# Kernel optimization log

Hardware: AMD Instinct MI355X
Metric: run time of the kernel (lower is better)

Reference implementation:

```python
import jax, jax.numpy as jnp
import numpy as np

N_NODES = 50000
N_EDGES = 1600000
D_IN = 128
D_HID = 128
D_OUT = 128


def setup_inputs() -> dict:
    key = jax.random.key(0)
    ks = jax.random.split(key, 12)
    s = 0.05
    return {
        "x": jax.random.normal(ks[0], (N_NODES, D_IN), jnp.float32),
        "src": jax.random.randint(ks[1], (N_EDGES,), 0, N_NODES),
        "dst": jax.random.randint(ks[2], (N_EDGES,), 0, N_NODES),
        "W_neigh1": jax.random.normal(ks[3], (D_HID, D_IN), jnp.float32) * s,
        "W_self1": jax.random.normal(ks[4], (D_HID, D_IN), jnp.float32) * s,
        "b_self1": jnp.zeros((D_HID,), jnp.float32),
        "W_neigh2": jax.random.normal(ks[5], (D_HID, D_HID), jnp.float32) * s,
        "W_self2": jax.random.normal(ks[6], (D_HID, D_HID), jnp.float32) * s,
        "b_self2": jnp.zeros((D_HID,), jnp.float32),
        "W_neigh3": jax.random.normal(ks[7], (D_OUT, D_HID), jnp.float32) * s,
        "W_self3": jax.random.normal(ks[8], (D_OUT, D_HID), jnp.float32) * s,
        "b_self3": jnp.zeros((D_OUT,), jnp.float32),
    }


def _sage_mean(h, src, dst, inv_deg, W_neigh, W_self, b_self):
    # DGL SAGEConv 'mean': fc_self(h) + fc_neigh(mean of in-neighbor feats)
    # zero in-degree nodes get zero neighbor term (inv_deg = 0 there is avoided
    # by clamping degree to >=1, sum is 0 anyway).
    neigh_sum = jax.ops.segment_sum(h[src], dst, num_segments=h.shape[0])  # [N, d]
    h_neigh = neigh_sum * inv_deg  # [N, d]
    return h @ W_self.T + b_self + h_neigh @ W_neigh.T


def reference(x, src, dst, W_neigh1, W_self1, b_self1, W_neigh2, W_self2, b_self2, W_neigh3, W_self3, b_self3):
    n = x.shape[0]
    deg = jax.ops.segment_sum(jnp.ones((src.shape[0],), x.dtype), dst, num_segments=n)
    inv_deg = (1.0 / jnp.maximum(deg, 1.0))[:, None]  # [N, 1]
    h = jax.nn.relu(_sage_mean(x, src, dst, inv_deg, W_neigh1, W_self1, b_self1))
    h = jax.nn.relu(_sage_mean(h, src, dst, inv_deg, W_neigh2, W_self2, b_self2))
    h = _sage_mean(h, src, dst, inv_deg, W_neigh3, W_self3, b_self3)
    return h
```

## Files before the change

kernel.cpp:

```cpp
#include <hip/hip_runtime.h>


constexpr int N_NODES = 50000;
constexpr int N_EDGES = 1600000;
constexpr int D = 128;

constexpr int NBUCK = 392;
constexpr int BCAP  = 6144;
constexpr int EPB   = 4096;
constexpr int CS_BLOCKS = (N_EDGES + EPB - 1) / EPB;
constexpr int GC_STRIDE = 16;

constexpr int NT  = 8;
constexpr int TSH = 13;

typedef __bf16 bf16x8 __attribute__((ext_vector_type(8)));
typedef float f32x4 __attribute__((ext_vector_type(4)));
union U8 { bf16x8 v; __bf16 e[8]; };

__global__ void zero1(int* __restrict__ a, int n) {
    int i = blockIdx.x * blockDim.x + threadIdx.x;
    if (i < n) a[i] = 0;
}

__global__ __launch_bounds__(256) void bucket_count_scatter(
        const int* __restrict__ dst, const int* __restrict__ src,
        int* __restrict__ gcursor, int* __restrict__ bucketbuf) {
    __shared__ int hcnt[NBUCK];
    __shared__ int hbase[NBUCK];
    const int tid = threadIdx.x;
    for (int i = tid; i < NBUCK; i += 256) hcnt[i] = 0;
    __syncthreads();

    const int e0 = blockIdx.x * EPB;
    int d[16], lp[16];
    #pragma unroll
    for (int t = 0; t < 16; ++t) {
        const int e = e0 + t * 256 + tid;
        if (e < N_EDGES) {
            d[t] = dst[e];
            lp[t] = atomicAdd(&hcnt[d[t] >> 7], 1);
        } else {
            d[t] = 0; lp[t] = -1;
        }
    }
    __syncthreads();

    for (int i = tid; i < NBUCK; i += 256) {
        const int c = hcnt[i];
        hbase[i] = c ? atomicAdd(&gcursor[i * GC_STRIDE], c) : 0;
    }
    __syncthreads();

    #pragma unroll
    for (int t = 0; t < 16; ++t) {
        const int e = e0 + t * 256 + tid;
        if (e < N_EDGES) {
            const int s  = src[e];
            const int bk = d[t] >> 7;
            const int p  = hbase[bk] + lp[t];
            if (p < BCAP)
                bucketbuf[bk * BCAP + p] = ((d[t] & 127) << 16) | s;
        }
    }
}

__global__ void bucket_scan(const int* __restrict__ gcursor,
                            int* __restrict__ bucket_base) {
    __shared__ int wsum[8], wpre[8];
    const int t = threadIdx.x;
    const int lane = t & 63, w = t >> 6;
    int v = 0;
    if (t < NBUCK) { v = gcursor[t * GC_STRIDE]; if (v > BCAP) v = BCAP; }
    int x = v;
    #pragma unroll
    for (int off = 1; off < 64; off <<= 1) {
        int tt = __shfl_up(x, off, 64);
        if (lane >= off) x += tt;
    }
    if (lane == 63) wsum[w] = x;
    __syncthreads();
    if (t < 8) {
        int s = wsum[t], y = s;
        #pragma unroll
        for (int off = 1; off < 8; off <<= 1) {
            int tt = __shfl_up(y, off, 64);
            if (t >= off) y += tt;
        }
        wpre[t] = y - s;
    }
    __syncthreads();
    if (t < NBUCK) bucket_base[t] = wpre[w] + (x - v);
}

__global__ __launch_bounds__(256) void bucket_csr(
        const int* __restrict__ gcursor, const int* __restrict__ bucket_base,
        const int* __restrict__ bucketbuf, int* __restrict__ tp,
        float* __restrict__ inv_deg, int* __restrict__ esrc) {
    __shared__ int h[1024];
    __shared__ int cur[1024];
    __shared__ int wsum[4], wpre[4];
    const int bk = blockIdx.x, tid = threadIdx.x;
    int cnt = gcursor[bk * GC_STRIDE];
    if (cnt > BCAP) cnt = BCAP;
    const int base = bucket_base[bk];
    #pragma unroll
    for (int k = 0; k < 4; ++k) h[tid * 4 + k] = 0;
    __syncthreads();

    const int* bb = bucketbuf + (size_t)bk * BCAP;
    for (int i = tid; i < cnt; i += 256) {
        const int p = bb[i];
        atomicAdd(&h[((p >> 16) << 3) | ((p & 0xFFFF) >> TSH)], 1);
    }
    __syncthreads();

    if (tid < 128) {
        int dg = 0;
        #pragma unroll
        for (int k = 0; k < 8; ++k) dg += h[tid * 8 + k];
        inv_deg[bk * 128 + tid] = 1.0f / fmaxf((float)dg, 1.0f);
    }

    const int v0 = h[tid * 4], v1 = h[tid * 4 + 1];
    const int v2 = h[tid * 4 + 2], v3 = h[tid * 4 + 3];
    const int s = v0 + v1 + v2 + v3;
    int x = s;
    const int lane = tid & 63, w = tid >> 6;
    #pragma unroll
    for (int off = 1; off < 64; off <<= 1) {
        int tt = __shfl_up(x, off, 64);
        if (lane >= off) x += tt;
    }
    if (lane == 63) wsum[w] = x;
    __syncthreads();
    if (tid == 0) {
        int a = 0;
        #pragma unroll
        for (int k = 0; k < 4; ++k) { wpre[k] = a; a += wsum[k]; }
    }
    __syncthreads();
    const int e0 = wpre[w] + (x - s);
    const int e1 = e0 + v0, e2 = e1 + v1, e3 = e2 + v2;
    cur[tid * 4] = e0; cur[tid * 4 + 1] = e1;
    cur[tid * 4 + 2] = e2; cur[tid * 4 + 3] = e3;
    int* tpo = tp + (size_t)bk * 1024 + tid * 4;
    tpo[0] = base + e0; tpo[1] = base + e1; tpo[2] = base + e2; tpo[3] = base + e3;
    __syncthreads();

    for (int i = tid; i < cnt; i += 256) {
        const int p = bb[i];
        const int f = ((p >> 16) << 3) | ((p & 0xFFFF) >> TSH);
        esrc[base + atomicAdd(&cur[f], 1)] = p & 0xFFFF;
    }
}

__global__ void pack_w(const float* __restrict__ w0, const float* __restrict__ w1,
                       const float* __restrict__ w2, const float* __restrict__ w3,
                       const float* __restrict__ w4, const float* __restrict__ w5,
                       __bf16* __restrict__ outbase) {
    const float* ws[6] = {w0, w1, w2, w3, w4, w5};
    const float* W = ws[blockIdx.y];
    __bf16* o = outbase + (size_t)blockIdx.y * 32768;
    int idx = blockIdx.x * 256 + threadIdx.x;
    int t = idx & 7;
    int lane = (idx >> 3) & 63;
    int ks = (idx >> 9) & 3;
    int jt = idx >> 11;
    int j = jt * 16 + (lane & 15);
    int k = ks * 32 + (lane >> 4) * 8 + t;
    float w = W[j * D + k];
    __bf16 hi = (__bf16)w;
    o[idx] = hi;
    o[16384 + idx] = (__bf16)(w - (float)hi);
}

__global__ __launch_bounds__(256) void dual_gemm(
        const float* __restrict__ h, const __bf16* __restrict__ Bs,
        const __bf16* __restrict__ Bn, const float* __restrict__ bias,
        float* __restrict__ y_self, __bf16* __restrict__ z) {
    const int wave = threadIdx.x >> 6;
    const int lane = threadIdx.x & 63;
    const int tile = blockIdx.x * 4 + wave;
    if (tile >= N_NODES / 16) return;
    const int n0 = tile * 16;
    const int row = n0 + (lane & 15);
    const int koff = (lane >> 4) * 8;

    U8 ahi[4], alo[4];
    #pragma unroll
    for (int ks = 0; ks < 4; ++ks) {
        const float* p = h + (size_t)row * D + ks * 32 + koff;
        float f[8];
        *(f32x4*)&f[0] = *(const f32x4*)p;
        *(f32x4*)&f[4] = *(const f32x4*)(p + 4);
        #pragma unroll
        for (int t = 0; t < 8; ++t) {
            __bf16 hi = (__bf16)f[t];
            ahi[ks].e[t] = hi;
            alo[ks].e[t] = (__bf16)(f[t] - (float)hi);
        }
    }

    const int jcol = lane & 15;
    const int r0 = (lane >> 4) * 4;

    #pragma unroll 2
    for (int jt = 0; jt < 8; ++jt) {
        f32x4 accS = {0.f, 0.f, 0.f, 0.f};
        f32x4 accN = {0.f, 0.f, 0.f, 0.f};
        #pragma unroll
        for (int ks = 0; ks < 4; ++ks) {
            const size_t off = (((size_t)jt * 4 + ks) * 64 + lane) * 8;
            bf16x8 wsh = *(const bf16x8*)(Bs + off);
            bf16x8 wsl = *(const bf16x8*)(Bs + 16384 + off);
            bf16x8 wnh = *(const bf16x8*)(Bn + off);
            bf16x8 wnl = *(const bf16x8*)(Bn + 16384 + off);
            accS = __builtin_amdgcn_mfma_f32_16x16x32_bf16(ahi[ks].v, wsh, accS, 0, 0, 0);
            accS = __builtin_amdgcn_mfma_f32_16x16x32_bf16(alo[ks].v, wsh, accS, 0, 0, 0);
            accS = __builtin_amdgcn_mfma_f32_16x16x32_bf16(ahi[ks].v, wsl, accS, 0, 0, 0);
            accN = __builtin_amdgcn_mfma_f32_16x16x32_bf16(ahi[ks].v, wnh, accN, 0, 0, 0);
            accN = __builtin_amdgcn_mfma_f32_16x16x32_bf16(alo[ks].v, wnh, accN, 0, 0, 0);
            accN = __builtin_amdgcn_mfma_f32_16x16x32_bf16(ahi[ks].v, wnl, accN, 0, 0, 0);
        }
        const int j = jt * 16 + jcol;
        const float bj = bias[j];
        #pragma unroll
        for (int r = 0; r < 4; ++r) {
            const size_t n = n0 + r0 + r;
            y_self[n * D + j] = accS[r] + bj;
            z[n * D + j] = (__bf16)accN[r];
        }
    }
}

__global__ __launch_bounds__(256) void agg_add(
        const __bf16* __restrict__ z, const int* __restrict__ esrc,
        const int* __restrict__ tp, const float* __restrict__ inv_deg,
        const float* __restrict__ y_self, float* __restrict__ out, int do_relu) {
    const int n = blockIdx.x * 4 + (threadIdx.x >> 6);
    const int lane = threadIdx.x & 63;
    const int s = lane >> 4;
    const int c = lane & 15;
    const int r0 = tp[n * NT], r1 = tp[(n + 1) * NT];

    float acc[8] = {0.f, 0.f, 0.f, 0.f, 0.f, 0.f, 0.f, 0.f};
    int e = r0 + s;
    for (; e + 12 < r1; e += 16) {
        int i0 = esrc[e], i1 = esrc[e + 4], i2 = esrc[e + 8], i3 = esrc[e + 12];
        U8 v0, v1, v2, v3;
        v0.v = *(const bf16x8*)(z + (size_t)i0 * D + c * 8);
        v1.v = *(const bf16x8*)(z + (size_t)i1 * D + c * 8);
        v2.v = *(const bf16x8*)(z + (size_t)i2 * D + c * 8);
        v3.v = *(const bf16x8*)(z + (size_t)i3 * D + c * 8);
        #pragma unroll
        for (int t = 0; t < 8; ++t)
            acc[t] += ((float)v0.e[t] + (float)v1.e[t]) + ((float)v2.e[t] + (float)v3.e[t]);
    }
    for (; e < r1; e += 4) {
        U8 v0;
        v0.v = *(const bf16x8*)(z + (size_t)esrc[e] * D + c * 8);
        #pragma unroll
        for (int t = 0; t < 8; ++t) acc[t] += (float)v0.e[t];
    }
    #pragma unroll
    for (int t = 0; t < 8; ++t) acc[t] += __shfl_down(acc[t], 32, 64);
    #pragma unroll
    for (int t = 0; t < 8; ++t) acc[t] += __shfl_down(acc[t], 16, 64);

    if (lane < 16) {
        const float idg = inv_deg[n];
        const float* yp = y_self + (size_t)n * D + c * 8;
        f32x4 y0 = *(const f32x4*)yp;
        f32x4 y1 = *(const f32x4*)(yp + 4);
        float o[8];
        #pragma unroll
        for (int t = 0; t < 4; ++t) o[t] = y0[t] + acc[t] * idg;
        #pragma unroll
        for (int t = 0; t < 4; ++t) o[4 + t] = y1[t] + acc[4 + t] * idg;
        if (do_relu) {
            #pragma unroll
            for (int t = 0; t < 8; ++t) o[t] = fmaxf(o[t], 0.f);
        }
        float* op = out + (size_t)n * D + c * 8;
        *(f32x4*)op = *(f32x4*)&o[0];
        *(f32x4*)(op + 4) = *(f32x4*)&o[4];
    }
}

extern "C" void kernel_launch(void* const* d_in, const int* in_sizes, int n_in,
                              void* d_out, int out_size, void* d_ws, size_t ws_size,
                              hipStream_t stream) {
    const float* x   = (const float*)d_in[0];
    const int* src   = (const int*)d_in[1];
    const int* dst   = (const int*)d_in[2];
    const float* Wn1 = (const float*)d_in[3];
    const float* Ws1 = (const float*)d_in[4];
    const float* b1  = (const float*)d_in[5];
    const float* Wn2 = (const float*)d_in[6];
    const float* Ws2 = (const float*)d_in[7];
    const float* b2  = (const float*)d_in[8];
    const float* Wn3 = (const float*)d_in[9];
    const float* Ws3 = (const float*)d_in[10];
    const float* b3  = (const float*)d_in[11];
    float* out = (float*)d_out;

    char* w = (char*)d_ws;
    float* inv_deg     = (float*)w;             w += 50176 * 4;
    int* tp            = (int*)w;               w += (size_t)NBUCK * 1024 * 4;
    int* gcursor       = (int*)w;               w += NBUCK * GC_STRIDE * 4;
    int* bucket_base   = (int*)w;               w += 512 * 4;
    int* esrc          = (int*)w;               w += (size_t)N_EDGES * 4;
    __bf16* Bpk        = (__bf16*)w;            w += 6 * 32768 * 2;
    __bf16* zbuf       = (__bf16*)w;            w += (size_t)50176 * D * 2;
    float* bufA        = (float*)w;

    int* bucketbuf = (int*)zbuf;

    const __bf16* PWs1 = Bpk + 0 * 32768, *PWn1 = Bpk + 1 * 32768;
    const __bf16* PWs2 = Bpk + 2 * 32768, *PWn2 = Bpk + 3 * 32768;
    const __bf16* PWs3 = Bpk + 4 * 32768, *PWn3 = Bpk + 5 * 32768;

    zero1<<<(NBUCK * GC_STRIDE + 255) / 256, 256, 0, stream>>>(gcursor, NBUCK * GC_STRIDE);
    bucket_count_scatter<<<CS_BLOCKS, 256, 0, stream>>>(dst, src, gcursor, bucketbuf);
    bucket_scan<<<1, 512, 0, stream>>>(gcursor, bucket_base);
    bucket_csr<<<NBUCK, 256, 0, stream>>>(gcursor, bucket_base, bucketbuf,
                                          tp, inv_deg, esrc);

    pack_w<<<dim3(64, 6), 256, 0, stream>>>(Ws1, Wn1, Ws2, Wn2, Ws3, Wn3, Bpk);

    const int ggrid = (N_NODES / 16 + 3) / 4;
    const int agrid = N_NODES / 4;

    dual_gemm<<<ggrid, 256, 0, stream>>>(x, PWs1, PWn1, b1, bufA, zbuf);
    agg_add<<<agrid, 256, 0, stream>>>(zbuf, esrc, tp, inv_deg, bufA, bufA, 1);

    dual_gemm<<<ggrid, 256, 0, stream>>>(bufA, PWs2, PWn2, b2, out, zbuf);
    agg_add<<<agrid, 256, 0, stream>>>(zbuf, esrc, tp, inv_deg, out, out, 1);

    dual_gemm<<<ggrid, 256, 0, stream>>>(out, PWs3, PWn3, b3, bufA, zbuf);
    agg_add<<<agrid, 256, 0, stream>>>(zbuf, esrc, tp, inv_deg, bufA, out, 0);
}
```

Baseline: 380.7 us.

## Aggregate-then-transform with bf16 hi/lo planes and fold bucket scan into CSR

Reorders each layer so the mean aggregation runs first on a bf16 feature plane, then one fused GEMM computes the self and neighbour products, adds bias, applies relu and writes hi/lo bf16 planes for the next layer. This removes the fp32 y_self round trip and the separate add pass. The bucket scan kernel is replaced by a per-block prefix reduction inside bucket_csr, and the zero kernel by a memset. In exchange it adds a split_x pass, the aggregation gathers only the hi bf16 plane, which loses precision, and the mean is stored as two extra planes.

```diff
diff --git a/kernel.cpp b/kernel.cpp
--- a/kernel.cpp
+++ b/kernel.cpp
@@ -4,6 +4,7 @@
 constexpr int N_NODES = 50000;
 constexpr int N_EDGES = 1600000;
 constexpr int D = 128;
+constexpr int NTILES = N_NODES / 16;
 
 constexpr int NBUCK = 392;
 constexpr int BCAP  = 6144;
@@ -17,11 +18,6 @@
 typedef __bf16 bf16x8 __attribute__((ext_vector_type(8)));
 typedef float f32x4 __attribute__((ext_vector_type(4)));
 union U8 { bf16x8 v; __bf16 e[8]; };
-
-__global__ void zero1(int* __restrict__ a, int n) {
-    int i = blockIdx.x * blockDim.x + threadIdx.x;
-    if (i < n) a[i] = 0;
-}
 
 __global__ __launch_bounds__(256) void bucket_count_scatter(
         const int* __restrict__ dst, const int* __restrict__ src,
@@ -65,48 +61,31 @@
     }
 }
 
-__global__ void bucket_scan(const int* __restrict__ gcursor,
-                            int* __restrict__ bucket_base) {
-    __shared__ int wsum[8], wpre[8];
-    const int t = threadIdx.x;
-    const int lane = t & 63, w = t >> 6;
-    int v = 0;
-    if (t < NBUCK) { v = gcursor[t * GC_STRIDE]; if (v > BCAP) v = BCAP; }
-    int x = v;
-    #pragma unroll
-    for (int off = 1; off < 64; off <<= 1) {
-        int tt = __shfl_up(x, off, 64);
-        if (lane >= off) x += tt;
-    }
-    if (lane == 63) wsum[w] = x;
-    __syncthreads();
-    if (t < 8) {
-        int s = wsum[t], y = s;
-        #pragma unroll
-        for (int off = 1; off < 8; off <<= 1) {
-            int tt = __shfl_up(y, off, 64);
-            if (t >= off) y += tt;
-        }
-        wpre[t] = y - s;
-    }
-    __syncthreads();
-    if (t < NBUCK) bucket_base[t] = wpre[w] + (x - v);
-}
-
 __global__ __launch_bounds__(256) void bucket_csr(
-        const int* __restrict__ gcursor, const int* __restrict__ bucket_base,
-        const int* __restrict__ bucketbuf, int* __restrict__ tp,
-        float* __restrict__ inv_deg, int* __restrict__ esrc) {
+        const int* __restrict__ gcursor, const int* __restrict__ bucketbuf,
+        int* __restrict__ tp, float* __restrict__ inv_deg,
+        int* __restrict__ esrc) {
     __shared__ int h[1024];
     __shared__ int cur[1024];
     __shared__ int wsum[4], wpre[4];
+    __shared__ int redw[4];
     const int bk = blockIdx.x, tid = threadIdx.x;
     int cnt = gcursor[bk * GC_STRIDE];
     if (cnt > BCAP) cnt = BCAP;
-    const int base = bucket_base[bk];
+
+    int partial = 0;
+    for (int i = tid; i < bk; i += 256) {
+        int v = gcursor[i * GC_STRIDE];
+        partial += (v > BCAP ? BCAP : v);
+    }
+    #pragma unroll
+    for (int off = 32; off; off >>= 1) partial += __shfl_down(partial, off, 64);
+    if ((tid & 63) == 0) redw[tid >> 6] = partial;
+
     #pragma unroll
     for (int k = 0; k < 4; ++k) h[tid * 4 + k] = 0;
     __syncthreads();
+    const int base = redw[0] + redw[1] + redw[2] + redw[3];
 
     const int* bb = bucketbuf + (size_t)bk * BCAP;
     for (int i = tid; i < cnt; i += 256) {
@@ -175,69 +154,24 @@
     o[16384 + idx] = (__bf16)(w - (float)hi);
 }
 
-__global__ __launch_bounds__(256) void dual_gemm(
-        const float* __restrict__ h, const __bf16* __restrict__ Bs,
-        const __bf16* __restrict__ Bn, const float* __restrict__ bias,
-        float* __restrict__ y_self, __bf16* __restrict__ z) {
-    const int wave = threadIdx.x >> 6;
-    const int lane = threadIdx.x & 63;
-    const int tile = blockIdx.x * 4 + wave;
-    if (tile >= N_NODES / 16) return;
-    const int n0 = tile * 16;
-    const int row = n0 + (lane & 15);
-    const int koff = (lane >> 4) * 8;
-
-    U8 ahi[4], alo[4];
-    #pragma unroll
-    for (int ks = 0; ks < 4; ++ks) {
-        const float* p = h + (size_t)row * D + ks * 32 + koff;
-        float f[8];
-        *(f32x4*)&f[0] = *(const f32x4*)p;
-        *(f32x4*)&f[4] = *(const f32x4*)(p + 4);
-        #pragma unroll
-        for (int t = 0; t < 8; ++t) {
-            __bf16 hi = (__bf16)f[t];
-            ahi[ks].e[t] = hi;
-            alo[ks].e[t] = (__bf16)(f[t] - (float)hi);
-        }
-    }
-
-    const int jcol = lane & 15;
-    const int r0 = (lane >> 4) * 4;
-
-    #pragma unroll 2
-    for (int jt = 0; jt < 8; ++jt) {
-        f32x4 accS = {0.f, 0.f, 0.f, 0.f};
-        f32x4 accN = {0.f, 0.f, 0.f, 0.f};
-        #pragma unroll
-        for (int ks = 0; ks < 4; ++ks) {
-            const size_t off = (((size_t)jt * 4 + ks) * 64 + lane) * 8;
-            bf16x8 wsh = *(const bf16x8*)(Bs + off);
-            bf16x8 wsl = *(const bf16x8*)(Bs + 16384 + off);
-            bf16x8 wnh = *(const bf16x8*)(Bn + off);
-            bf16x8 wnl = *(const bf16x8*)(Bn + 16384 + off);
-            accS = __builtin_amdgcn_mfma_f32_16x16x32_bf16(ahi[ks].v, wsh, accS, 0, 0, 0);
-            accS = __builtin_amdgcn_mfma_f32_16x16x32_bf16(alo[ks].v, wsh, accS, 0, 0, 0);
-            accS = __builtin_amdgcn_mfma_f32_16x16x32_bf16(ahi[ks].v, wsl, accS, 0, 0, 0);
-            accN = __builtin_amdgcn_mfma_f32_16x16x32_bf16(ahi[ks].v, wnh, accN, 0, 0, 0);
-            accN = __builtin_amdgcn_mfma_f32_16x16x32_bf16(alo[ks].v, wnh, accN, 0, 0, 0);
-            accN = __builtin_amdgcn_mfma_f32_16x16x32_bf16(ahi[ks].v, wnl, accN, 0, 0, 0);
-        }
-        const int j = jt * 16 + jcol;
-        const float bj = bias[j];
-        #pragma unroll
-        for (int r = 0; r < 4; ++r) {
-            const size_t n = n0 + r0 + r;
-            y_self[n * D + j] = accS[r] + bj;
-            z[n * D + j] = (__bf16)accN[r];
-        }
-    }
-}
-
-__global__ __launch_bounds__(256) void agg_add(
-        const __bf16* __restrict__ z, const int* __restrict__ esrc,
+__global__ __launch_bounds__(256) void split_x(const float* __restrict__ x,
+                                               __bf16* __restrict__ xh, int n8) {
+    const int i = blockIdx.x * 256 + threadIdx.x;
+    if (i < n8) {
+        const float* p = x + (size_t)i * 8;
+        const f32x4 a = *(const f32x4*)p;
+        const f32x4 b = *(const f32x4*)(p + 4);
+        U8 h;
+        #pragma unroll
+        for (int k = 0; k < 4; ++k) { h.e[k] = (__bf16)a[k]; h.e[4 + k] = (__bf16)b[k]; }
+        *(bf16x8*)(xh + (size_t)i * 8) = h.v;
+    }
+}
+
+__global__ __launch_bounds__(256) void agg_mean(
+        const __bf16* __restrict__ hplane, const int* __restrict__ esrc,
         const int* __restrict__ tp, const float* __restrict__ inv_deg,
-        const float* __restrict__ y_self, float* __restrict__ out, int do_relu) {
+        __bf16* __restrict__ m_hi, __bf16* __restrict__ m_lo) {
     const int n = blockIdx.x * 4 + (threadIdx.x >> 6);
     const int lane = threadIdx.x & 63;
     const int s = lane >> 4;
@@ -249,17 +183,17 @@
     for (; e + 12 < r1; e += 16) {
         int i0 = esrc[e], i1 = esrc[e + 4], i2 = esrc[e + 8], i3 = esrc[e + 12];
         U8 v0, v1, v2, v3;
-        v0.v = *(const bf16x8*)(z + (size_t)i0 * D + c * 8);
-        v1.v = *(const bf16x8*)(z + (size_t)i1 * D + c * 8);
-        v2.v = *(const bf16x8*)(z + (size_t)i2 * D + c * 8);
-        v3.v = *(const bf16x8*)(z + (size_t)i3 * D + c * 8);
+        v0.v = *(const bf16x8*)(hplane + (size_t)i0 * D + c * 8);
+        v1.v = *(const bf16x8*)(hplane + (size_t)i1 * D + c * 8);
+        v2.v = *(const bf16x8*)(hplane + (size_t)i2 * D + c * 8);
+        v3.v = *(const bf16x8*)(hplane + (size_t)i3 * D + c * 8);
         #pragma unroll
         for (int t = 0; t < 8; ++t)
             acc[t] += ((float)v0.e[t] + (float)v1.e[t]) + ((float)v2.e[t] + (float)v3.e[t]);
     }
     for (; e < r1; e += 4) {
         U8 v0;
-        v0.v = *(const bf16x8*)(z + (size_t)esrc[e] * D + c * 8);
+        v0.v = *(const bf16x8*)(hplane + (size_t)esrc[e] * D + c * 8);
         #pragma unroll
         for (int t = 0; t < 8; ++t) acc[t] += (float)v0.e[t];
     }
@@ -270,21 +204,102 @@
 
     if (lane < 16) {
         const float idg = inv_deg[n];
-        const float* yp = y_self + (size_t)n * D + c * 8;
-        f32x4 y0 = *(const f32x4*)yp;
-        f32x4 y1 = *(const f32x4*)(yp + 4);
-        float o[8];
-        #pragma unroll
-        for (int t = 0; t < 4; ++t) o[t] = y0[t] + acc[t] * idg;
-        #pragma unroll
-        for (int t = 0; t < 4; ++t) o[4 + t] = y1[t] + acc[4 + t] * idg;
-        if (do_relu) {
+        U8 mh, ml;
+        #pragma unroll
+        for (int t = 0; t < 8; ++t) {
+            const float mm = acc[t] * idg;
+            const __bf16 hi = (__bf16)mm;
+            mh.e[t] = hi;
+            ml.e[t] = (__bf16)(mm - (float)hi);
+        }
+        *(bf16x8*)(m_hi + (size_t)n * D + c * 8) = mh.v;
+        *(bf16x8*)(m_lo + (size_t)n * D + c * 8) = ml.v;
+    }
+}
+
+__global__ __launch_bounds__(256) void fused_gemm(
+        const float* __restrict__ x32,
+        const __bf16* __restrict__ a_hi, const __bf16* __restrict__ a_lo,
+        const __bf16* __restrict__ m_hi, const __bf16* __restrict__ m_lo,
+        const __bf16* __restrict__ Bs, const __bf16* __restrict__ Bn,
+        const float* __restrict__ bias,
+        __bf16* __restrict__ o_hi, __bf16* __restrict__ o_lo,
+        float* __restrict__ o32) {
+    const int wave = threadIdx.x >> 6;
+    const int lane = threadIdx.x & 63;
+    const int tile = blockIdx.x * 4 + wave;
+    if (tile >= NTILES) return;
+    const int n0 = tile * 16;
+    const int row = n0 + (lane & 15);
+    const int koff = (lane >> 4) * 8;
+
+    U8 ah[4], al[4], mh[4], ml[4];
+    if (x32) {
+        #pragma unroll
+        for (int ks = 0; ks < 4; ++ks) {
+            const float* p = x32 + (size_t)row * D + ks * 32 + koff;
+            float f[8];
+            *(f32x4*)&f[0] = *(const f32x4*)p;
+            *(f32x4*)&f[4] = *(const f32x4*)(p + 4);
             #pragma unroll
-            for (int t = 0; t < 8; ++t) o[t] = fmaxf(o[t], 0.f);
-        }
-        float* op = out + (size_t)n * D + c * 8;
-        *(f32x4*)op = *(f32x4*)&o[0];
-        *(f32x4*)(op + 4) = *(f32x4*)&o[4];
+            for (int t = 0; t < 8; ++t) {
+                const __bf16 hi = (__bf16)f[t];
+                ah[ks].e[t] = hi;
+                al[ks].e[t] = (__bf16)(f[t] - (float)hi);
+            }
+        }
+    } else {
+        #pragma unroll
+        for (int ks = 0; ks < 4; ++ks) {
+            ah[ks].v = *(const bf16x8*)(a_hi + (size_t)row * D + ks * 32 + koff);
+            al[ks].v = *(const bf16x8*)(a_lo + (size_t)row * D + ks * 32 + koff);
+        }
+    }
+    #pragma unroll
+    for (int ks = 0; ks < 4; ++ks) {
+        mh[ks].v = *(const bf16x8*)(m_hi + (size_t)row * D + ks * 32 + koff);
+        ml[ks].v = *(const bf16x8*)(m_lo + (size_t)row * D + ks * 32 + koff);
+    }
+
+    const int jcol = lane & 15;
+    const int r0q = (lane >> 4) * 4;
+
+    #pragma unroll 2
+    for (int jt = 0; jt < 8; ++jt) {
+        f32x4 accS = {0.f, 0.f, 0.f, 0.f};
+        f32x4 accN = {0.f, 0.f, 0.f, 0.f};
+        #pragma unroll
+        for (int ks = 0; ks < 4; ++ks) {
+            const size_t off = (((size_t)jt * 4 + ks) * 64 + lane) * 8;
+            const bf16x8 wsh = *(const bf16x8*)(Bs + off);
+            const bf16x8 wsl = *(const bf16x8*)(Bs + 16384 + off);
+            const bf16x8 wnh = *(const bf16x8*)(Bn + off);
+            const bf16x8 wnl = *(const bf16x8*)(Bn + 16384 + off);
+            accS = __builtin_amdgcn_mfma_f32_16x16x32_bf16(ah[ks].v, wsh, accS, 0, 0, 0);
+            accS = __builtin_amdgcn_mfma_f32_16x16x32_bf16(al[ks].v, wsh, accS, 0, 0, 0);
+            accS = __builtin_amdgcn_mfma_f32_16x16x32_bf16(ah[ks].v, wsl, accS, 0, 0, 0);
+            accN = __builtin_amdgcn_mfma_f32_16x16x32_bf16(mh[ks].v, wnh, accN, 0, 0, 0);
+            accN = __builtin_amdgcn_mfma_f32_16x16x32_bf16(ml[ks].v, wnh, accN, 0, 0, 0);
+            accN = __builtin_amdgcn_mfma_f32_16x16x32_bf16(mh[ks].v, wnl, accN, 0, 0, 0);
+        }
+        const int j = jt * 16 + jcol;
+        const float bj = bias[j];
+        if (o32) {
+            #pragma unroll
+            for (int r = 0; r < 4; ++r) {
+                const size_t n = n0 + r0q + r;
+                o32[n * D + j] = accS[r] + accN[r] + bj;
+            }
+        } else {
+            #pragma unroll
+            for (int r = 0; r < 4; ++r) {
+                const size_t n = n0 + r0q + r;
+                float o = fmaxf(accS[r] + accN[r] + bj, 0.f);
+                const __bf16 hi = (__bf16)o;
+                o_hi[n * D + j] = hi;
+                o_lo[n * D + j] = (__bf16)(o - (float)hi);
+            }
+        }
     }
 }
 
@@ -305,39 +320,47 @@
     const float* b3  = (const float*)d_in[11];
     float* out = (float*)d_out;
 
+    constexpr size_t PLANE = (size_t)50176 * D * 2;
+
     char* w = (char*)d_ws;
-    float* inv_deg     = (float*)w;             w += 50176 * 4;
-    int* tp            = (int*)w;               w += (size_t)NBUCK * 1024 * 4;
-    int* gcursor       = (int*)w;               w += NBUCK * GC_STRIDE * 4;
-    int* bucket_base   = (int*)w;               w += 512 * 4;
-    int* esrc          = (int*)w;               w += (size_t)N_EDGES * 4;
-    __bf16* Bpk        = (__bf16*)w;            w += 6 * 32768 * 2;
-    __bf16* zbuf       = (__bf16*)w;            w += (size_t)50176 * D * 2;
-    float* bufA        = (float*)w;
-
-    int* bucketbuf = (int*)zbuf;
+    float* inv_deg = (float*)w;                 w += 50176 * 4;
+    int* tp        = (int*)w;                   w += (size_t)NBUCK * 1024 * 4;
+    int* gcursor   = (int*)w;                   w += NBUCK * GC_STRIDE * 4;
+    int* esrc      = (int*)w;                   w += (size_t)N_EDGES * 4;
+    __bf16* Bpk    = (__bf16*)w;                w += 6 * 32768 * 2;
+    __bf16* xh     = (__bf16*)w;                w += PLANE;
+    __bf16* mhi    = (__bf16*)w;                w += PLANE;
+    __bf16* mlo    = (__bf16*)w;                w += PLANE;
+    __bf16* pAh    = (__bf16*)w;                w += PLANE;
+    __bf16* pAl    = (__bf16*)w;                w += PLANE;
+    __bf16* pBh    = (__bf16*)w;                w += PLANE;
+    __bf16* pBl    = (__bf16*)w;
+
+    int* bucketbuf = (int*)pBh;
 
     const __bf16* PWs1 = Bpk + 0 * 32768, *PWn1 = Bpk + 1 * 32768;
     const __bf16* PWs2 = Bpk + 2 * 32768, *PWn2 = Bpk + 3 * 32768;
     const __bf16* PWs3 = Bpk + 4 * 32768, *PWn3 = Bpk + 5 * 32768;
 
-    zero1<<<(NBUCK * GC_STRIDE + 255) / 256, 256, 0, stream>>>(gcursor, NBUCK * GC_STRIDE);
+    hipMemsetAsync(gcursor, 0, NBUCK * GC_STRIDE * 4, stream);
     bucket_count_scatter<<<CS_BLOCKS, 256, 0, stream>>>(dst, src, gcursor, bucketbuf);
-    bucket_scan<<<1, 512, 0, stream>>>(gcursor, bucket_base);
-    bucket_csr<<<NBUCK, 256, 0, stream>>>(gcursor, bucket_base, bucketbuf,
-                                          tp, inv_deg, esrc);
+    bucket_csr<<<NBUCK, 256, 0, stream>>>(gcursor, bucketbuf, tp, inv_deg, esrc);
 
     pack_w<<<dim3(64, 6), 256, 0, stream>>>(Ws1, Wn1, Ws2, Wn2, Ws3, Wn3, Bpk);
-
-    const int ggrid = (N_NODES / 16 + 3) / 4;
+    split_x<<<(N_NODES * D / 8 + 255) / 256, 256, 0, stream>>>(x, xh, N_NODES * D / 8);
+
+    const int ggrid = (NTILES + 3) / 4;
     const int agrid = N_NODES / 4;
 
-    dual_gemm<<<ggrid, 256, 0, stream>>>(x, PWs1, PWn1, b1, bufA, zbuf);
-    agg_add<<<agrid, 256, 0, stream>>>(zbuf, esrc, tp, inv_deg, bufA, bufA, 1);
-
-    dual_gemm<<<ggrid, 256, 0, stream>>>(bufA, PWs2, PWn2, b2, out, zbuf);
-    agg_add<<<agrid, 256, 0, stream>>>(zbuf, esrc, tp, inv_deg, out, out, 1);
-
-    dual_gemm<<<ggrid, 256, 0, stream>>>(out, PWs3, PWn3, b3, bufA, zbuf);
-    agg_add<<<agrid, 256, 0, stream>>>(zbuf, esrc, tp, inv_deg, bufA, out, 0);
-}
+    agg_mean<<<agrid, 256, 0, stream>>>(xh, esrc, tp, inv_deg, mhi, mlo);
+    fused_gemm<<<ggrid, 256, 0, stream>>>(x, nullptr, nullptr, mhi, mlo,
+                                          PWs1, PWn1, b1, pAh, pAl, nullptr);
+
+    agg_mean<<<agrid, 256, 0, stream>>>(pAh, esrc, tp, inv_deg, mhi, mlo);
+    fused_gemm<<<ggrid, 256, 0, stream>>>(nullptr, pAh, pAl, mhi, mlo,
+                                          PWs2, PWn2, b2, pBh, pBl, nullptr);
+
+    agg_mean<<<agrid, 256, 0, stream>>>(pBh, esrc, tp, inv_deg, mhi, mlo);
+    fused_gemm<<<ggrid, 256, 0, stream>>>(nullptr, pBh, pBl, mhi, mlo,
+                                          PWs3, PWn3, b3, nullptr, nullptr, out);
+}
```

Result: no change. 386.3 us (+1.5%).
